# Kernel optimization log

Measured on AMD Instinct MI355X. Metric: run time of the kernel, lower is better.

Reference implementation:

```python
import jax, jax.numpy as jnp
import numpy as np

E = 8          # node_emb_dim (number of LSTM ensembles)
H = 128        # fixed_lstm_hidden
D = 8          # feature dim
CONT = 168     # cont_len (encoder length)
HORIZON = 24   # decoder length
T = CONT + HORIZON
B = 4096       # batch of node ids
NUM_TS = 4096


def _lstm(xs, W, U, b, h0, c0):
    """Time-major LSTM (Keras gate order i,f,g,o). xs: [T,B,in]. Returns final (h,c) and all hs."""
    def step(carry, x):
        h, c = carry
        z = x @ W + h @ U + b                      # [B, 4H]
        i, f, g, o = jnp.split(z, 4, axis=-1)
        i = jax.nn.sigmoid(i)
        f = jax.nn.sigmoid(f)
        g = jnp.tanh(g)
        o = jax.nn.sigmoid(o)
        c = f * c + i * g
        h = o * jnp.tanh(c)
        return (h, c), h
    (h, c), hs = jax.lax.scan(step, (h0, c0), xs)
    return h, c, hs


def setup_inputs() -> dict:
    key = jax.random.key(0)
    ks = jax.random.split(key, 12)
    s = 0.05  # small init scale to keep LSTM gates unsaturated
    return {
        "feats": jax.random.normal(ks[0], (T, D), jnp.float32),
        "y_prev": jax.random.normal(ks[1], (CONT, B), jnp.float32),
        "nid": jax.random.randint(ks[2], (B,), 0, NUM_TS, jnp.int32),
        "emb_table": jax.random.uniform(ks[3], (NUM_TS, E), jnp.float32),
        "enc_W": jax.random.normal(ks[4], (E, 1 + D, 4 * H), jnp.float32) * s,
        "enc_U": jax.random.normal(ks[5], (E, H, 4 * H), jnp.float32) * s,
        "enc_b": jnp.zeros((E, 4 * H), jnp.float32),
        "dec_W": jax.random.normal(ks[6], (E, D, 4 * H), jnp.float32) * s,
        "dec_U": jax.random.normal(ks[7], (E, H, 4 * H), jnp.float32) * s,
        "dec_b": jnp.zeros((E, 4 * H), jnp.float32),
        "out_w": jax.random.normal(ks[8], (E, H), jnp.float32) * s,
    }


def reference(feats, y_prev, nid, emb_table, enc_W, enc_U, enc_b, dec_W, dec_U, dec_b, out_w):
    cont_len = y_prev.shape[0]
    b = nid.shape[0]
    # normalized node embedding: abs then row-normalize, then lookup
    embs = jnp.abs(emb_table)
    embs = embs / jnp.sum(embs, axis=1, keepdims=True)
    node_emb = embs[nid]                                   # [B, E]
    # broadcast features over batch (time-major)
    feats_b = jnp.broadcast_to(feats[:, None, :], (feats.shape[0], b, feats.shape[1]))
    enc_inp = jnp.concatenate([y_prev[..., None], feats_b[:cont_len]], axis=-1)  # [CONT,B,1+D]
    feats_futr = feats_b[cont_len:]                        # [HOR,B,D]
    hdim = enc_U.shape[1]
    h0 = jnp.zeros((b, hdim), feats.dtype)
    c0 = jnp.zeros((b, hdim), feats.dtype)

    def run_one(eW, eU, eb, dW, dU, db, ow):
        h, c, _ = _lstm(enc_inp, eW, eU, eb, h0, c0)
        _, _, hs = _lstm(feats_futr, dW, dU, db, h, c)     # [HOR,B,H]
        return jnp.einsum('tbh,h->tb', hs, ow)             # Dense(1, no bias) -> [HOR,B]

    outs = jax.vmap(run_one)(enc_W, enc_U, enc_b, dec_W, dec_U, dec_b, out_w)  # [E,HOR,B]
    fixed_effect = jnp.einsum('etb,be->tb', outs, node_emb)                    # [HOR,B]
    return fixed_effect
```

## Files before the change

### kernel.cpp

```cpp
#include <hip/hip_runtime.h>
#include <stdint.h>

#define NE 8
#define NH 128
#define ND 8
#define NCONT 168
#define NHOR 24
#define NB 4096
#define NG 512
#define BT 64

typedef float f32x4 __attribute__((ext_vector_type(4)));
typedef short bf16x8 __attribute__((ext_vector_type(8)));

__device__ __forceinline__ unsigned short f2bf(float f){
  union { float f; unsigned u; } v; v.f = f;
  unsigned r = (v.u + 0x7FFFu + ((v.u >> 16) & 1u)) >> 16;
  return (unsigned short)r;
}
__device__ __forceinline__ float bf2f(unsigned short s){
  union { unsigned u; float f; } v; v.u = ((unsigned)s) << 16; return v.f;
}
__device__ __forceinline__ float sigm(float x){
  return __builtin_amdgcn_rcpf(1.0f + __builtin_amdgcn_exp2f(-1.44269504f * x));
}
__device__ __forceinline__ float tanh_fast(float x){
  return 1.0f - 2.0f * __builtin_amdgcn_rcpf(1.0f + __builtin_amdgcn_exp2f(2.88539008f * x));
}

__global__ void prep_fxw_enc(const float* __restrict__ feats, const float* __restrict__ W,
                             const float* __restrict__ bias, float* __restrict__ out){
  int idx = blockIdx.x * blockDim.x + threadIdx.x;
  if (idx >= NE * NCONT * NG) return;
  int j = idx & (NG - 1);
  int t = (idx >> 9) % NCONT;
  int e = idx / (NCONT * NG);
  float s = bias[e * NG + j];
  #pragma unroll
  for (int i = 0; i < ND; ++i)
    s += feats[t * ND + i] * W[(e * 9 + 1 + i) * NG + j];
  out[idx] = s;
}

__global__ void prep_fxw_dec(const float* __restrict__ feats, const float* __restrict__ W,
                             const float* __restrict__ bias, float* __restrict__ out){
  int idx = blockIdx.x * blockDim.x + threadIdx.x;
  if (idx >= NE * NHOR * NG) return;
  int j = idx & (NG - 1);
  int t = (idx >> 9) % NHOR;
  int e = idx / (NHOR * NG);
  float s = bias[e * NG + j];
  #pragma unroll
  for (int i = 0; i < ND; ++i)
    s += feats[(NCONT + t) * ND + i] * W[(e * ND + i) * NG + j];
  out[idx] = s;
}

__global__ void prep_node(const int* __restrict__ nid, const float* __restrict__ emb,
                          float* __restrict__ node_w){
  int b = blockIdx.x * blockDim.x + threadIdx.x;
  if (b >= NB) return;
  int n = nid[b];
  float a[NE]; float s = 0.f;
  #pragma unroll
  for (int e = 0; e < NE; ++e){ a[e] = fabsf(emb[n * NE + e]); s += a[e]; }
  float inv = 1.0f / s;
  #pragma unroll
  for (int e = 0; e < NE; ++e) node_w[b * NE + e] = a[e] * inv;
}

__global__ __launch_bounds__(512, 2) void lstm_main(
    const float* __restrict__ y_prev,
    const float* __restrict__ enc_W,
    const float* __restrict__ enc_U,
    const float* __restrict__ dec_U,
    const float* __restrict__ out_w,
    const float* __restrict__ fxw_enc,
    const float* __restrict__ fxw_dec,
    float* __restrict__ ws_out)
{
  __shared__ unsigned short hl[2][BT * NH];
  __shared__ float ow_lds[NH];

  const int tid  = threadIdx.x;
  const int lane = tid & 63;
  const int w    = tid >> 6;
  const int e    = blockIdx.x & 7;
  const int b0   = (blockIdx.x >> 3) * BT;
  const int l15  = lane & 15;
  const int l4   = lane >> 4;
  const int kcol = w * 16 + l15;

  {
    f32x4 z4 = {0.f, 0.f, 0.f, 0.f};
    ((f32x4*)&hl[0][0])[tid]       = z4;
    ((f32x4*)&hl[0][0])[tid + 512] = z4;
    if (tid < NH) ow_lds[tid] = out_w[e * NH + tid];
  }

  bf16x8 uf[4][4];
  {
    const float* Ug = enc_U + e * NH * NG;
    #pragma unroll
    for (int g = 0; g < 4; ++g)
      #pragma unroll
      for (int kc = 0; kc < 4; ++kc){
        const float* p = Ug + (kc * 32 + l4 * 8) * NG + g * NH + kcol;
        bf16x8 v;
        #pragma unroll
        for (int j = 0; j < 8; ++j) v[j] = (short)f2bf(p[j * NG]);
        uf[g][kc] = v;
      }
  }

  float w0[4];
  #pragma unroll
  for (int g = 0; g < 4; ++g) w0[g] = enc_W[e * 9 * NG + g * NH + kcol];

  float c_s[4][4];
  #pragma unroll
  for (int mf = 0; mf < 4; ++mf)
    #pragma unroll
    for (int rg = 0; rg < 4; ++rg) c_s[mf][rg] = 0.f;

  __syncthreads();

  int cur = 0;

  for (int t = 0; t < NCONT; ++t){
    f32x4 acc[4][4];
    #pragma unroll
    for (int mf = 0; mf < 4; ++mf)
      #pragma unroll
      for (int g = 0; g < 4; ++g) acc[mf][g] = (f32x4){0.f,0.f,0.f,0.f};

    #pragma unroll
    for (int kc = 0; kc < 4; ++kc){
      bf16x8 af[4];
      #pragma unroll
      for (int mf = 0; mf < 4; ++mf){
        int row = mf * 16 + l15;
        int eo  = (row * NH + kc * 32 + l4 * 8) ^ ((row & 7) << 3);
        af[mf] = *(const bf16x8*)&hl[cur][eo];
      }
      #pragma unroll
      for (int mf = 0; mf < 4; ++mf)
        #pragma unroll
        for (int g = 0; g < 4; ++g)
          acc[mf][g] = __builtin_amdgcn_mfma_f32_16x16x32_bf16(af[mf], uf[g][kc], acc[mf][g], 0, 0, 0);
    }

    const float* fx = fxw_enc + (e * NCONT + t) * NG;
    float fxv[4];
    #pragma unroll
    for (int g = 0; g < 4; ++g) fxv[g] = fx[g * NH + kcol];

    int nxt = cur ^ 1;
    #pragma unroll
    for (int mf = 0; mf < 4; ++mf){
      f32x4 yv = *(const f32x4*)&y_prev[t * NB + b0 + mf * 16 + l4 * 4];
      #pragma unroll
      for (int rg = 0; rg < 4; ++rg){
        float y  = yv[rg];
        float zi = acc[mf][0][rg] + fxv[0] + y * w0[0];
        float zf = acc[mf][1][rg] + fxv[1] + y * w0[1];
        float zg = acc[mf][2][rg] + fxv[2] + y * w0[2];
        float zo = acc[mf][3][rg] + fxv[3] + y * w0[3];
        float gi = sigm(zi), gf = sigm(zf);
        float gg = tanh_fast(zg), go = sigm(zo);
        float c  = gf * c_s[mf][rg] + gi * gg;
        c_s[mf][rg] = c;
        float h  = go * tanh_fast(c);
        int r = mf * 16 + l4 * 4 + rg;
        hl[nxt][(r * NH + kcol) ^ ((r & 7) << 3)] = f2bf(h);
      }
    }
    cur = nxt;
    __syncthreads();
  }

  {
    const float* Ug = dec_U + e * NH * NG;
    #pragma unroll
    for (int g = 0; g < 4; ++g)
      #pragma unroll
      for (int kc = 0; kc < 4; ++kc){
        const float* p = Ug + (kc * 32 + l4 * 8) * NG + g * NH + kcol;
        bf16x8 v;
        #pragma unroll
        for (int j = 0; j < 8; ++j) v[j] = (short)f2bf(p[j * NG]);
        uf[g][kc] = v;
      }
  }

  for (int t = 0; t < NHOR; ++t){
    f32x4 acc[4][4];
    #pragma unroll
    for (int mf = 0; mf < 4; ++mf)
      #pragma unroll
      for (int g = 0; g < 4; ++g) acc[mf][g] = (f32x4){0.f,0.f,0.f,0.f};

    #pragma unroll
    for (int kc = 0; kc < 4; ++kc){
      bf16x8 af[4];
      #pragma unroll
      for (int mf = 0; mf < 4; ++mf){
        int row = mf * 16 + l15;
        int eo  = (row * NH + kc * 32 + l4 * 8) ^ ((row & 7) << 3);
        af[mf] = *(const bf16x8*)&hl[cur][eo];
      }
      #pragma unroll
      for (int mf = 0; mf < 4; ++mf)
        #pragma unroll
        for (int g = 0; g < 4; ++g)
          acc[mf][g] = __builtin_amdgcn_mfma_f32_16x16x32_bf16(af[mf], uf[g][kc], acc[mf][g], 0, 0, 0);
    }

    const float* fx = fxw_dec + (e * NHOR + t) * NG;
    float fxv[4];
    #pragma unroll
    for (int g = 0; g < 4; ++g) fxv[g] = fx[g * NH + kcol];

    int nxt = cur ^ 1;
    #pragma unroll
    for (int mf = 0; mf < 4; ++mf){
      #pragma unroll
      for (int rg = 0; rg < 4; ++rg){
        float zi = acc[mf][0][rg] + fxv[0];
        float zf = acc[mf][1][rg] + fxv[1];
        float zg = acc[mf][2][rg] + fxv[2];
        float zo = acc[mf][3][rg] + fxv[3];
        float gi = sigm(zi), gf = sigm(zf);
        float gg = tanh_fast(zg), go = sigm(zo);
        float c  = gf * c_s[mf][rg] + gi * gg;
        c_s[mf][rg] = c;
        float h  = go * tanh_fast(c);
        int r = mf * 16 + l4 * 4 + rg;
        hl[nxt][(r * NH + kcol) ^ ((r & 7) << 3)] = f2bf(h);
      }
    }
    cur = nxt;
    __syncthreads();

    int r  = w * 8 + (lane >> 3);
    int kg = (lane & 7) * 16;
    int e0 = (r * NH + kg)     ^ ((r & 7) << 3);
    int e1 = (r * NH + kg + 8) ^ ((r & 7) << 3);
    bf16x8 ha = *(const bf16x8*)&hl[cur][e0];
    bf16x8 hb = *(const bf16x8*)&hl[cur][e1];
    float s = 0.f;
    #pragma unroll
    for (int j = 0; j < 8; ++j){
      s += bf2f((unsigned short)ha[j]) * ow_lds[kg + j];
      s += bf2f((unsigned short)hb[j]) * ow_lds[kg + 8 + j];
    }
    s += __shfl_xor(s, 1);
    s += __shfl_xor(s, 2);
    s += __shfl_xor(s, 4);
    if ((lane & 7) == 0) ws_out[(e * NHOR + t) * NB + b0 + r] = s;
  }
}

__global__ void finalize(const float* __restrict__ ws_out, const float* __restrict__ node_w,
                         float* __restrict__ out){
  int idx = blockIdx.x * blockDim.x + threadIdx.x;
  if (idx >= NHOR * NB) return;
  int b = idx & (NB - 1);
  float s = 0.f;
  #pragma unroll
  for (int e = 0; e < NE; ++e)
    s += ws_out[e * NHOR * NB + idx] * node_w[b * NE + e];
  out[idx] = s;
}

extern "C" void kernel_launch(void* const* d_in, const int* in_sizes, int n_in,
                              void* d_out, int out_size, void* d_ws, size_t ws_size,
                              hipStream_t stream) {
  const float* feats  = (const float*)d_in[0];
  const float* y_prev = (const float*)d_in[1];
  const int*   nid    = (const int*)  d_in[2];
  const float* emb    = (const float*)d_in[3];
  const float* enc_W  = (const float*)d_in[4];
  const float* enc_U  = (const float*)d_in[5];
  const float* enc_b  = (const float*)d_in[6];
  const float* dec_W  = (const float*)d_in[7];
  const float* dec_U  = (const float*)d_in[8];
  const float* dec_b  = (const float*)d_in[9];
  const float* out_w  = (const float*)d_in[10];
  float* out = (float*)d_out;

  float* ws      = (float*)d_ws;
  float* fxw_enc = ws;
  float* fxw_dec = fxw_enc + NE * NCONT * NG;
  float* node_w  = fxw_dec + NE * NHOR * NG;
  float* ws_out  = node_w + NB * NE;

  prep_fxw_enc<<<(NE * NCONT * NG + 255) / 256, 256, 0, stream>>>(feats, enc_W, enc_b, fxw_enc);
  prep_fxw_dec<<<(NE * NHOR * NG + 255) / 256, 256, 0, stream>>>(feats, dec_W, dec_b, fxw_dec);
  prep_node<<<(NB + 255) / 256, 256, 0, stream>>>(nid, emb, node_w);
  lstm_main<<<NE * (NB / BT), 512, 0, stream>>>(y_prev, enc_W, enc_U, dec_U, out_w,
                                                fxw_enc, fxw_dec, ws_out);
  finalize<<<(NHOR * NB + 255) / 256, 256, 0, stream>>>(ws_out, node_w, out);
}
```

Baseline: 1.338 ms.

## Transpose LSTM MFMA operands, fold input bias into accumulator, pack bf16 stores

```diff
diff --git a/kernel.cpp b/kernel.cpp
--- a/kernel.cpp
+++ b/kernel.cpp
@@ -1,5 +1,6 @@
 #include <hip/hip_runtime.h>
 #include <stdint.h>
+#include <type_traits>
 
 #define NE 8
 #define NH 128
@@ -12,14 +13,17 @@
 
 typedef float f32x4 __attribute__((ext_vector_type(4)));
 typedef short bf16x8 __attribute__((ext_vector_type(8)));
+typedef unsigned int u32x2 __attribute__((ext_vector_type(2)));
 
 __device__ __forceinline__ unsigned short f2bf(float f){
   union { float f; unsigned u; } v; v.f = f;
   unsigned r = (v.u + 0x7FFFu + ((v.u >> 16) & 1u)) >> 16;
   return (unsigned short)r;
 }
-__device__ __forceinline__ float bf2f(unsigned short s){
-  union { unsigned u; float f; } v; v.u = ((unsigned)s) << 16; return v.f;
+__device__ __forceinline__ unsigned cvt_pk_bf16(float lo, float hi){
+  unsigned r;
+  asm("v_cvt_pk_bf16_f32 %0, %1, %2" : "=v"(r) : "v"(lo), "v"(hi));
+  return r;
 }
 __device__ __forceinline__ float sigm(float x){
   return __builtin_amdgcn_rcpf(1.0f + __builtin_amdgcn_exp2f(-1.44269504f * x));
@@ -80,7 +84,7 @@
     float* __restrict__ ws_out)
 {
   __shared__ unsigned short hl[2][BT * NH];
-  __shared__ float ow_lds[NH];
+  __shared__ float part[2][BT][9];
 
   const int tid  = threadIdx.x;
   const int lane = tid & 63;
@@ -89,175 +93,166 @@
   const int b0   = (blockIdx.x >> 3) * BT;
   const int l15  = lane & 15;
   const int l4   = lane >> 4;
-  const int kcol = w * 16 + l15;
+  const int hc0  = w * 16 + l4 * 4;
+
+  const int q   = (l15 >> 2) & 1;
+  const int Ae  = l15 * 128 + ((l4 ^ (l15 & 3)) << 3);
+  const int rb0 = 2 * (Ae + q * 32);
+  const int rb1 = 2 * (Ae + (1 - q) * 32);
+  const int wb  = 2 * ((l15 * 128 + hc0) ^ ((l15 & 7) << 3));
 
   {
     f32x4 z4 = {0.f, 0.f, 0.f, 0.f};
     ((f32x4*)&hl[0][0])[tid]       = z4;
     ((f32x4*)&hl[0][0])[tid + 512] = z4;
-    if (tid < NH) ow_lds[tid] = out_w[e * NH + tid];
-  }
-
-  bf16x8 uf[4][4];
+  }
+
+  bf16x8 ut[4][4];
   {
-    const float* Ug = enc_U + e * NH * NG;
+    const float* Ub = enc_U + e * NH * NG + w * 16 + l15;
     #pragma unroll
     for (int g = 0; g < 4; ++g)
       #pragma unroll
       for (int kc = 0; kc < 4; ++kc){
-        const float* p = Ug + (kc * 32 + l4 * 8) * NG + g * NH + kcol;
+        const float* p = Ub + (kc * 32 + l4 * 8) * NG + g * NH;
         bf16x8 v;
         #pragma unroll
         for (int j = 0; j < 8; ++j) v[j] = (short)f2bf(p[j * NG]);
-        uf[g][kc] = v;
-      }
-  }
-
-  float w0[4];
-  #pragma unroll
-  for (int g = 0; g < 4; ++g) w0[g] = enc_W[e * 9 * NG + g * NH + kcol];
-
-  float c_s[4][4];
-  #pragma unroll
-  for (int mf = 0; mf < 4; ++mf)
-    #pragma unroll
-    for (int rg = 0; rg < 4; ++rg) c_s[mf][rg] = 0.f;
+        ut[g][kc] = v;
+      }
+  }
+
+  f32x4 w04[4];
+  #pragma unroll
+  for (int g = 0; g < 4; ++g)
+    w04[g] = *(const f32x4*)&enc_W[(e * 9) * NG + g * NH + hc0];
+
+  float cs[4][4];
+  #pragma unroll
+  for (int nf = 0; nf < 4; ++nf)
+    #pragma unroll
+    for (int rg = 0; rg < 4; ++rg) cs[nf][rg] = 0.f;
+
+  const float* fxe = fxw_enc + e * NCONT * NG;
+  const float* yp  = y_prev + b0;
 
   __syncthreads();
 
-  int cur = 0;
-
-  for (int t = 0; t < NCONT; ++t){
+  auto step = [&](auto Bc, auto ENCc, const float* fxptr, float* pout){
+    constexpr int  B   = decltype(Bc)::value;
+    constexpr bool ENC = decltype(ENCc)::value;
+
+    f32x4 fxv[4];
+    #pragma unroll
+    for (int g = 0; g < 4; ++g) fxv[g] = *(const f32x4*)&fxptr[g * NH + hc0];
+    float yv[4];
+    if (ENC){
+      #pragma unroll
+      for (int nf = 0; nf < 4; ++nf) yv[nf] = yp[nf * 16 + l15];
+    }
+
     f32x4 acc[4][4];
     #pragma unroll
-    for (int mf = 0; mf < 4; ++mf)
-      #pragma unroll
-      for (int g = 0; g < 4; ++g) acc[mf][g] = (f32x4){0.f,0.f,0.f,0.f};
-
-    #pragma unroll
     for (int kc = 0; kc < 4; ++kc){
-      bf16x8 af[4];
-      #pragma unroll
-      for (int mf = 0; mf < 4; ++mf){
-        int row = mf * 16 + l15;
-        int eo  = (row * NH + kc * 32 + l4 * 8) ^ ((row & 7) << 3);
-        af[mf] = *(const bf16x8*)&hl[cur][eo];
-      }
-      #pragma unroll
-      for (int mf = 0; mf < 4; ++mf)
-        #pragma unroll
-        for (int g = 0; g < 4; ++g)
-          acc[mf][g] = __builtin_amdgcn_mfma_f32_16x16x32_bf16(af[mf], uf[g][kc], acc[mf][g], 0, 0, 0);
-    }
-
-    const float* fx = fxw_enc + (e * NCONT + t) * NG;
-    float fxv[4];
-    #pragma unroll
-    for (int g = 0; g < 4; ++g) fxv[g] = fx[g * NH + kcol];
-
-    int nxt = cur ^ 1;
-    #pragma unroll
-    for (int mf = 0; mf < 4; ++mf){
-      f32x4 yv = *(const f32x4*)&y_prev[t * NB + b0 + mf * 16 + l4 * 4];
+      bf16x8 hb[4];
+      #pragma unroll
+      for (int nf = 0; nf < 4; ++nf)
+        hb[nf] = *(const bf16x8*)((const char*)hl +
+                   (B * 16384 + nf * 4096 + (kc >> 1) * 128) + ((kc & 1) ? rb1 : rb0));
+      #pragma unroll
+      for (int nf = 0; nf < 4; ++nf)
+        #pragma unroll
+        for (int g = 0; g < 4; ++g){
+          if (kc == 0)
+            acc[nf][g] = __builtin_amdgcn_mfma_f32_16x16x32_bf16(ut[g][0], hb[nf], fxv[g], 0, 0, 0);
+          else
+            acc[nf][g] = __builtin_amdgcn_mfma_f32_16x16x32_bf16(ut[g][kc], hb[nf], acc[nf][g], 0, 0, 0);
+        }
+    }
+
+    #pragma unroll
+    for (int nf = 0; nf < 4; ++nf){
+      float hh[4];
       #pragma unroll
       for (int rg = 0; rg < 4; ++rg){
-        float y  = yv[rg];
-        float zi = acc[mf][0][rg] + fxv[0] + y * w0[0];
-        float zf = acc[mf][1][rg] + fxv[1] + y * w0[1];
-        float zg = acc[mf][2][rg] + fxv[2] + y * w0[2];
-        float zo = acc[mf][3][rg] + fxv[3] + y * w0[3];
+        float zi = acc[nf][0][rg];
+        float zf = acc[nf][1][rg];
+        float zg = acc[nf][2][rg];
+        float zo = acc[nf][3][rg];
+        if (ENC){
+          float y = yv[nf];
+          zi += y * w04[0][rg]; zf += y * w04[1][rg];
+          zg += y * w04[2][rg]; zo += y * w04[3][rg];
+        }
         float gi = sigm(zi), gf = sigm(zf);
         float gg = tanh_fast(zg), go = sigm(zo);
-        float c  = gf * c_s[mf][rg] + gi * gg;
-        c_s[mf][rg] = c;
-        float h  = go * tanh_fast(c);
-        int r = mf * 16 + l4 * 4 + rg;
-        hl[nxt][(r * NH + kcol) ^ ((r & 7) << 3)] = f2bf(h);
-      }
-    }
-    cur = nxt;
+        float c  = gf * cs[nf][rg] + gi * gg;
+        cs[nf][rg] = c;
+        hh[rg] = go * tanh_fast(c);
+      }
+      u32x2 pk;
+      pk.x = cvt_pk_bf16(hh[0], hh[1]);
+      pk.y = cvt_pk_bf16(hh[2], hh[3]);
+      *(u32x2*)((char*)hl + ((B ^ 1) * 16384 + nf * 4096) + wb) = pk;
+      if (!ENC) pout[nf] = hh[0]*pout[4] + hh[1]*pout[5] + hh[2]*pout[6] + hh[3]*pout[7];
+    }
     __syncthreads();
+  };
+
+  for (int t = 0; t < NCONT; t += 2){
+    step(std::integral_constant<int,0>{}, std::true_type{}, fxe, nullptr);
+    fxe += NG; yp += NB;
+    step(std::integral_constant<int,1>{}, std::true_type{}, fxe, nullptr);
+    fxe += NG; yp += NB;
   }
 
   {
-    const float* Ug = dec_U + e * NH * NG;
+    const float* Ub = dec_U + e * NH * NG + w * 16 + l15;
     #pragma unroll
     for (int g = 0; g < 4; ++g)
       #pragma unroll
       for (int kc = 0; kc < 4; ++kc){
-        const float* p = Ug + (kc * 32 + l4 * 8) * NG + g * NH + kcol;
+        const float* p = Ub + (kc * 32 + l4 * 8) * NG + g * NH;
         bf16x8 v;
         #pragma unroll
         for (int j = 0; j < 8; ++j) v[j] = (short)f2bf(p[j * NG]);
-        uf[g][kc] = v;
-      }
-  }
-
-  for (int t = 0; t < NHOR; ++t){
-    f32x4 acc[4][4];
-    #pragma unroll
-    for (int mf = 0; mf < 4; ++mf)
-      #pragma unroll
-      for (int g = 0; g < 4; ++g) acc[mf][g] = (f32x4){0.f,0.f,0.f,0.f};
-
-    #pragma unroll
-    for (int kc = 0; kc < 4; ++kc){
-      bf16x8 af[4];
-      #pragma unroll
-      for (int mf = 0; mf < 4; ++mf){
-        int row = mf * 16 + l15;
-        int eo  = (row * NH + kc * 32 + l4 * 8) ^ ((row & 7) << 3);
-        af[mf] = *(const bf16x8*)&hl[cur][eo];
-      }
-      #pragma unroll
-      for (int mf = 0; mf < 4; ++mf)
-        #pragma unroll
-        for (int g = 0; g < 4; ++g)
-          acc[mf][g] = __builtin_amdgcn_mfma_f32_16x16x32_bf16(af[mf], uf[g][kc], acc[mf][g], 0, 0, 0);
-    }
-
-    const float* fx = fxw_dec + (e * NHOR + t) * NG;
-    float fxv[4];
-    #pragma unroll
-    for (int g = 0; g < 4; ++g) fxv[g] = fx[g * NH + kcol];
-
-    int nxt = cur ^ 1;
-    #pragma unroll
-    for (int mf = 0; mf < 4; ++mf){
-      #pragma unroll
-      for (int rg = 0; rg < 4; ++rg){
-        float zi = acc[mf][0][rg] + fxv[0];
-        float zf = acc[mf][1][rg] + fxv[1];
-        float zg = acc[mf][2][rg] + fxv[2];
-        float zo = acc[mf][3][rg] + fxv[3];
-        float gi = sigm(zi), gf = sigm(zf);
-        float gg = tanh_fast(zg), go = sigm(zo);
-        float c  = gf * c_s[mf][rg] + gi * gg;
-        c_s[mf][rg] = c;
-        float h  = go * tanh_fast(c);
-        int r = mf * 16 + l4 * 4 + rg;
-        hl[nxt][(r * NH + kcol) ^ ((r & 7) << 3)] = f2bf(h);
-      }
-    }
-    cur = nxt;
-    __syncthreads();
-
-    int r  = w * 8 + (lane >> 3);
-    int kg = (lane & 7) * 16;
-    int e0 = (r * NH + kg)     ^ ((r & 7) << 3);
-    int e1 = (r * NH + kg + 8) ^ ((r & 7) << 3);
-    bf16x8 ha = *(const bf16x8*)&hl[cur][e0];
-    bf16x8 hb = *(const bf16x8*)&hl[cur][e1];
-    float s = 0.f;
-    #pragma unroll
-    for (int j = 0; j < 8; ++j){
-      s += bf2f((unsigned short)ha[j]) * ow_lds[kg + j];
-      s += bf2f((unsigned short)hb[j]) * ow_lds[kg + 8 + j];
-    }
-    s += __shfl_xor(s, 1);
-    s += __shfl_xor(s, 2);
-    s += __shfl_xor(s, 4);
-    if ((lane & 7) == 0) ws_out[(e * NHOR + t) * NB + b0 + r] = s;
+        ut[g][kc] = v;
+      }
+  }
+  f32x4 ow4 = *(const f32x4*)&out_w[e * NH + hc0];
+
+  const float* fxd = fxw_dec + e * NHOR * NG;
+
+  #pragma unroll 1
+  for (int td = 0; td < NHOR; td += 2){
+    #pragma unroll
+    for (int sub = 0; sub < 2; ++sub){
+      float pbuf[8];
+      pbuf[4] = ow4[0]; pbuf[5] = ow4[1]; pbuf[6] = ow4[2]; pbuf[7] = ow4[3];
+      if (sub == 0)
+        step(std::integral_constant<int,0>{}, std::false_type{}, fxd, pbuf);
+      else
+        step(std::integral_constant<int,1>{}, std::false_type{}, fxd, pbuf);
+      fxd += NG;
+      int t = td + sub;
+      int pb = t & 1;
+      #pragma unroll
+      for (int nf = 0; nf < 4; ++nf){
+        pbuf[nf] += __shfl_xor(pbuf[nf], 16);
+        pbuf[nf] += __shfl_xor(pbuf[nf], 32);
+      }
+      if (lane < 16){
+        #pragma unroll
+        for (int nf = 0; nf < 4; ++nf) part[pb][nf * 16 + l15][w] = pbuf[nf];
+      }
+      __syncthreads();
+      if (w == 0){
+        float s = 0.f;
+        #pragma unroll
+        for (int ww = 0; ww < 8; ++ww) s += part[pb][lane][ww];
+        ws_out[(e * NHOR + t) * NB + b0 + lane] = s;
+      }
+    }
   }
 }
 
```

Result: faster. 1.290 ms (-3.6%).
